# Performance work log

Measured on AMD Instinct MI355X. Metric: run time of the kernel, lower is better.

The kernel has to match this reference:

```python
import jax, jax.numpy as jnp
import numpy as np

T, B, D, H, L = 512, 64, 1024, 1024, 2
W_SCALE = 0.02  # keep tanh out of saturation


def setup_inputs() -> dict:
    key = jax.random.key(0)
    ks = jax.random.split(key, 7)
    return {
        "x": jax.random.normal(ks[0], (T, B, D), dtype=jnp.float32),
        "Wi": jax.random.normal(ks[1], (L, H, D), dtype=jnp.float32) * W_SCALE,
        "bi": jax.random.normal(ks[2], (L, H), dtype=jnp.float32) * W_SCALE,
        "Wh": jax.random.normal(ks[3], (L, H, H), dtype=jnp.float32) * W_SCALE,
        "bh": jax.random.normal(ks[4], (L, H), dtype=jnp.float32) * W_SCALE,
        "Wo": jax.random.normal(ks[5], (L, H, H), dtype=jnp.float32) * W_SCALE,
        "bo": jax.random.normal(ks[6], (L, H), dtype=jnp.float32) * W_SCALE,
    }


def reference(x, Wi, bi, Wh, bh, Wo, bo):
    # Faithful to the original: ONE hidden state shared across all layers,
    # overwritten by each RNNCell call within a timestep.
    num_layers = Wi.shape[0]
    batch = x.shape[1]
    hidden0 = jnp.zeros((batch, Wh.shape[-1]), dtype=x.dtype)

    def step(hidden, xt):
        out = xt
        for l in range(num_layers):
            # h = i2h(out) + h2h(hidden); o = h2o(h); new hidden = tanh(h)
            h = out @ Wi[l].T + bi[l] + hidden @ Wh[l].T + bh[l]  # [B,H]
            out = h @ Wo[l].T + bo[l]
            hidden = jnp.tanh(h)
        return hidden, out

    final_hidden, outs = jax.lax.scan(step, hidden0, x)  # outs: [T,B,H]
    return outs, final_hidden
```

## Files before the change

### kernel.cpp

```cpp
#include <hip/hip_runtime.h>
#include <cstdint>
#include <cstddef>

#define TT   512
#define NWG  256
#define SLOT 65536
#define SLOTB 262144
#define FINALOFF ((size_t)TT * (size_t)SLOT)

#define OFF_M     0
#define OFF_H0    2097152
#define OFF_TH0   (OFF_H0 + 131072)
#define OFF_TH1   (OFF_TH0 + 131072)
#define OFF_H1A   (OFF_TH1 + 131072)
#define OFF_H1B   (OFF_H1A + 131072)
#define OFF_B0    (OFF_H1B + 131072)
#define OFF_C1    (OFF_B0 + 4096)
#define OFF_FLAGS (OFF_C1 + 4096)

typedef _Float16 f16;
typedef unsigned long long ull;
typedef _Float16 v8h __attribute__((ext_vector_type(8)));
typedef float v4f __attribute__((ext_vector_type(4)));

union U2 { ull u[2]; v8h v; };
union P4 { f16 h[4]; ull u; };

__device__ __forceinline__ void st2(void* p, f16 v) {
  __hip_atomic_store((unsigned short*)p, __builtin_bit_cast(unsigned short, v),
                     __ATOMIC_RELAXED, __HIP_MEMORY_SCOPE_AGENT);
}
__device__ __forceinline__ ull ld8(const void* p) {
  return __hip_atomic_load((const ull*)p, __ATOMIC_RELAXED, __HIP_MEMORY_SCOPE_AGENT);
}
__device__ __forceinline__ void ld_frags(const f16* base, v8h out[8]) {
  ull u0[8], u1[8];
#pragma unroll
  for (int s = 0; s < 8; ++s) { const f16* p = base + s * 32; u0[s] = ld8(p); u1[s] = ld8(p + 4); }
#pragma unroll
  for (int s = 0; s < 8; ++s) { U2 c; c.u[0] = u0[s]; c.u[1] = u1[s]; out[s] = c.v; }
}

__device__ __forceinline__ float rcpf(float x) {
#if __has_builtin(__builtin_amdgcn_rcpf)
  return __builtin_amdgcn_rcpf(x);
#else
  return 1.0f / x;
#endif
}
__device__ __forceinline__ float tanhfast(float x) {
  x = fminf(fmaxf(x, -20.0f), 20.0f);
  const float u = __expf(-2.0f * x);
  return 1.0f - 2.0f * u * rcpf(1.0f + u);
}

__global__ void k_init(unsigned int* flags) {
  flags[threadIdx.x] = 0u;
}

__global__ void k_bias(const float* __restrict__ Wi, const float* __restrict__ bi,
                       const float* __restrict__ bh, const float* __restrict__ bo,
                       float* __restrict__ b0, float* __restrict__ c1) {
  const int i = blockIdx.x * 256 + threadIdx.x;
  const float* row = Wi + 1048576 + (size_t)i * 1024;
  float s = 0.f;
  for (int k = 0; k < 1024; k += 4) {
    const float4 w = *(const float4*)&row[k];
    const float4 v = *(const float4*)&bo[k];
    s += w.x * v.x + w.y * v.y + w.z * v.z + w.w * v.w;
  }
  c1[i] = s + bi[1024 + i] + bh[1024 + i];
  b0[i] = bi[i] + bh[i];
}

__global__ __launch_bounds__(256) void k_gemm_M(const float* __restrict__ Wi,
                                                const float* __restrict__ Wo,
                                                f16* __restrict__ Mh) {
  const float* A = Wi + 1048576;
  const float* B = Wo;
  __shared__ float As[16][68];
  __shared__ float Bs[16][68];
  const int bi = blockIdx.x >> 4, bj = blockIdx.x & 15;
  const int i0 = bi * 64, d0 = bj * 64;
  const int ti = threadIdx.x >> 4, tj = threadIdx.x & 15;
  float acc[4][4] = {};
  for (int kc = 0; kc < 1024; kc += 16) {
    const int r = threadIdx.x >> 2, cg = (threadIdx.x & 3) << 2;
    const float4 av = *(const float4*)&A[(size_t)(i0 + r) * 1024 + kc + cg];
    As[cg + 0][r] = av.x; As[cg + 1][r] = av.y; As[cg + 2][r] = av.z; As[cg + 3][r] = av.w;
    const int c2 = threadIdx.x >> 4, dg = (threadIdx.x & 15) << 2;
    const float4 bv = *(const float4*)&B[(size_t)(kc + c2) * 1024 + d0 + dg];
    *(float4*)&Bs[c2][dg] = bv;
    __syncthreads();
#pragma unroll
    for (int kk = 0; kk < 16; ++kk) {
      float a[4], b[4];
#pragma unroll
      for (int q = 0; q < 4; ++q) { a[q] = As[kk][ti * 4 + q]; b[q] = Bs[kk][tj * 4 + q]; }
#pragma unroll
      for (int p = 0; p < 4; ++p)
#pragma unroll
        for (int q = 0; q < 4; ++q) acc[p][q] += a[p] * b[q];
    }
    __syncthreads();
  }
#pragma unroll
  for (int p = 0; p < 4; ++p)
#pragma unroll
    for (int q = 0; q < 4; ++q)
      Mh[(size_t)(i0 + ti * 4 + p) * 1024 + (size_t)(d0 + tj * 4 + q)] = (f16)acc[p][q];
}

__global__ __launch_bounds__(256, 1) void k_z1(const float* __restrict__ x,
                                               const float* __restrict__ Wi,
                                               const float* __restrict__ b0p,
                                               float* __restrict__ dout) {
  const int t = blockIdx.x;
  const int tid = threadIdx.x, l = tid & 63, w = tid >> 6;
  const int lj = l & 15, lk = l >> 4;
  __shared__ __align__(16) f16 XL[64 * 1032];
  const float* xt = x + (size_t)t * SLOT;
  for (int u = tid; u < 16384; u += 256) {
    const int b = u >> 8, c4 = (u & 255) << 2;
    const float4 v = *(const float4*)&xt[(size_t)b * 1024 + c4];
    P4 p; p.h[0] = (f16)v.x; p.h[1] = (f16)v.y; p.h[2] = (f16)v.z; p.h[3] = (f16)v.w;
    *(ull*)&XL[b * 1032 + c4] = p.u;
  }
  __syncthreads();
  for (int jt = 0; jt < 16; ++jt) {
    const int jb = w * 256 + jt * 16;
    v4f acc[4] = {{0.f,0.f,0.f,0.f},{0.f,0.f,0.f,0.f},{0.f,0.f,0.f,0.f},{0.f,0.f,0.f,0.f}};
    for (int ks = 0; ks < 32; ++ks) {
      const int k0 = ks * 32 + lk * 8;
      const float* p = &Wi[(size_t)(jb + lj) * 1024 + k0];
      const float4 a = *(const float4*)p, b = *(const float4*)(p + 4);
      const v8h wf = {(f16)a.x,(f16)a.y,(f16)a.z,(f16)a.w,
                      (f16)b.x,(f16)b.y,(f16)b.z,(f16)b.w};
#pragma unroll
      for (int bt = 0; bt < 4; ++bt) {
        const v8h xf = *(const v8h*)&XL[(bt * 16 + lj) * 1032 + k0];
        acc[bt] = __builtin_amdgcn_mfma_f32_16x16x32_f16(xf, wf, acc[bt], 0, 0, 0);
      }
    }
    const float bias = b0p[jb + lj];
#pragma unroll
    for (int bt = 0; bt < 4; ++bt)
#pragma unroll
      for (int q = 0; q < 4; ++q) {
        const int b = bt * 16 + lk * 4 + q;
        f16* dst = (f16*)((char*)dout + (size_t)t * SLOTB + (size_t)(b >> 4) * 65536
                          + (size_t)(b & 15) * 2048) + (jb + lj);
        *dst = (f16)(acc[bt][q] + bias);
      }
  }
}

__global__ __launch_bounds__(256, 1) void k_rnn(
    const float* __restrict__ Wh, const float* __restrict__ Wo,
    const float* __restrict__ bo,
    char* __restrict__ ws, float* __restrict__ dout)
{
  const f16* Mh = (const f16*)(ws + OFF_M);
  f16* h0h  = (f16*)(ws + OFF_H0);
  f16* th0h = (f16*)(ws + OFF_TH0);
  f16* th1h = (f16*)(ws + OFF_TH1);
  f16* h1r[2] = { (f16*)(ws + OFF_H1A), (f16*)(ws + OFF_H1B) };
  const float* c1p = (const float*)(ws + OFF_C1);
  unsigned int* flags = (unsigned int*)(ws + OFF_FLAGS);

  const int wg = blockIdx.x;
  const int bq = wg & 3;
  const int jt = wg >> 2;
  const int j0 = jt * 16;
  const int tid = threadIdx.x;
  const int l = tid & 63, w = tid >> 6;
  const int lj = l & 15, lk = l >> 4;
  const int rb = tid >> 4, rj = tid & 15;
  unsigned int* gf = flags + bq * 64;

  __shared__ __align__(16) char WLb[4 * 32768];
  __shared__ float red[1024];

  {
    const float* srcs[3] = { Wh, Wh + 1048576, Wo + 1048576 };
    const int mi[3] = { 0, 2, 3 };
#pragma unroll
    for (int m = 0; m < 3; ++m) {
      const float* src = srcs[m];
      for (int u = tid; u < 4096; u += 256) {
        const int j = u >> 8, c4 = (u & 255) << 2;
        const float4 v = *(const float4*)&src[(size_t)(j0 + j) * 1024 + c4];
        P4 p; p.h[0] = (f16)v.x; p.h[1] = (f16)v.y; p.h[2] = (f16)v.z; p.h[3] = (f16)v.w;
        *(ull*)(WLb + mi[m] * 32768 + ((c4 >> 3) << 8) + (j << 4) + ((c4 & 4) << 1)) = p.u;
      }
    }
    for (int u = tid; u < 2048; u += 256) {
      const int j = u >> 7, c8 = (u & 127) << 3;
      const v8h mv = *(const v8h*)&Mh[(size_t)(j0 + j) * 1024 + c8];
      *(v8h*)(WLb + 32768 + ((c8 >> 3) << 8) + (j << 4)) = mv;
    }
  }
  const float c1v = c1p[j0 + rj];
  const float bo1v = bo[1024 + j0 + rj];
  __syncthreads();

  const size_t actbase = (size_t)(bq * 16 + lj) * 1024 + (size_t)(w * 256 + lk * 8);
  const int redw = w * 256 + lk * 64 + lj;
  const size_t rdst = (size_t)(bq * 16 + rb) * 1024 + (size_t)(j0 + rj);
  const int fbase = ((w * 32 + lk) << 8) + (lj << 4);

  auto wfrag = [&](int m, int s) -> v8h {
    return *(const v8h*)(WLb + m * 32768 + fbase + (s << 10));
  };
  auto zptr = [&](int t) -> const f16* {
    return (const f16*)((const char*)dout + (size_t)t * SLOTB + (size_t)bq * 65536
                        + (size_t)rb * 2048) + (j0 + rj);
  };
  auto reduce4 = [&](v4f a) -> float {
    __syncthreads();
#pragma unroll
    for (int q = 0; q < 4; ++q) red[redw + q * 16] = a[q];
    __syncthreads();
    return red[tid] + red[256 + tid] + red[512 + tid] + red[768 + tid];
  };
  auto arrive = [&](unsigned int ph) {
    asm volatile("s_waitcnt vmcnt(0)" ::: "memory");
    __syncthreads();
    if (tid == 0)
      __hip_atomic_store(&gf[jt], ph, __ATOMIC_RELAXED, __HIP_MEMORY_SCOPE_AGENT);
  };
  auto wait = [&](unsigned int ph) {
    if (tid < 64)
      while (__hip_atomic_load(&gf[tid], __ATOMIC_RELAXED, __HIP_MEMORY_SCOPE_AGENT) < ph)
        __builtin_amdgcn_s_sleep(1);
    __syncthreads();
    asm volatile("" ::: "memory");
  };

  float zv = (float)(*zptr(0));
  unsigned int ph = 0;
  v4f a2 = {0.f, 0.f, 0.f, 0.f};

  for (int t = 0; t < TT; ++t) {
    v8h hrf[8];
    v4f accA = {0.f, 0.f, 0.f, 0.f};
    if (t > 0) {
      v8h thf[8];
      ld_frags(th1h + actbase, thf);
      ld_frags(h1r[(t - 1) & 1] + actbase, hrf);
#pragma unroll
      for (int s = 0; s < 8; ++s)
        accA = __builtin_amdgcn_mfma_f32_16x16x32_f16(thf[s], wfrag(0, s), accA, 0, 0, 0);
    }
    const float h0 = reduce4(accA) + zv;
    st2(&h0h[rdst], (f16)h0);
    st2(&th0h[rdst], (f16)tanhfast(h0));
    arrive(++ph);
    float zn = 0.f;
    if (t + 1 < TT) zn = (float)(*zptr(t + 1));
    if (t > 0) {
      v4f aa = {0.f, 0.f, 0.f, 0.f};
#pragma unroll
      for (int s = 0; s < 8; ++s)
        aa = __builtin_amdgcn_mfma_f32_16x16x32_f16(hrf[s], wfrag(3, s), aa, 0, 0, 0);
      a2 = aa;
    }
    wait(ph);

    v8h g0f[8], t0f[8];
    ld_frags(h0h + actbase, g0f);
    ld_frags(th0h + actbase, t0f);
    v4f aM = {0.f, 0.f, 0.f, 0.f}, aW = {0.f, 0.f, 0.f, 0.f};
#pragma unroll
    for (int s = 0; s < 8; ++s) {
      aM = __builtin_amdgcn_mfma_f32_16x16x32_f16(g0f[s], wfrag(1, s), aM, 0, 0, 0);
      aW = __builtin_amdgcn_mfma_f32_16x16x32_f16(t0f[s], wfrag(2, s), aW, 0, 0, 0);
    }
    const float h1 = reduce4(aM + aW) + c1v;
    const float th1v = tanhfast(h1);
    st2(&h1r[t & 1][rdst], (f16)h1);
    st2(&th1h[rdst], (f16)th1v);
    if (t == TT - 1) dout[FINALOFF + rdst] = th1v;
    arrive(++ph);
    if (t > 0)
      dout[(size_t)(t - 1) * SLOT + rdst] = reduce4(a2) + bo1v;
    wait(ph);
    zv = zn;
  }

  {
    v8h hrf[8];
    ld_frags(h1r[(TT - 1) & 1] + actbase, hrf);
    v4f aa = {0.f, 0.f, 0.f, 0.f};
#pragma unroll
    for (int s = 0; s < 8; ++s)
      aa = __builtin_amdgcn_mfma_f32_16x16x32_f16(hrf[s], wfrag(3, s), aa, 0, 0, 0);
    dout[(size_t)(TT - 1) * SLOT + rdst] = reduce4(aa) + bo1v;
  }
}

extern "C" void kernel_launch(void* const* d_in, const int* in_sizes, int n_in,
                              void* d_out, int out_size, void* d_ws, size_t ws_size,
                              hipStream_t stream) {
  (void)in_sizes; (void)n_in; (void)out_size; (void)ws_size;
  const float* x  = (const float*)d_in[0];
  const float* Wi = (const float*)d_in[1];
  const float* bi = (const float*)d_in[2];
  const float* Wh = (const float*)d_in[3];
  const float* bh = (const float*)d_in[4];
  const float* Wo = (const float*)d_in[5];
  const float* bo = (const float*)d_in[6];
  char* ws = (char*)d_ws;
  float* out = (float*)d_out;

  k_init<<<1, 256, 0, stream>>>((unsigned int*)(ws + OFF_FLAGS));
  k_bias<<<4, 256, 0, stream>>>(Wi, bi, bh, bo, (float*)(ws + OFF_B0), (float*)(ws + OFF_C1));
  k_gemm_M<<<256, 256, 0, stream>>>(Wi, Wo, (f16*)(ws + OFF_M));
  k_z1<<<512, 256, 0, stream>>>(x, Wi, (const float*)(ws + OFF_B0), out);
  k_rnn<<<NWG, 256, 0, stream>>>(Wh, Wo, bo, ws, out);
}
```

Before: 6.255 ms.

## Repartition persistent RNN into 8-column tiles with counter barriers and blocked activations

Each workgroup now owns 8 hidden columns across two batch quarters instead of 16 columns of one quarter. The activation buffers move to a blocked layout so each tile's output is one contiguous 256-byte chunk. The per-workgroup flag array polled by 64 threads is replaced by atomic arrival counters polled by a single load. The aim is to cut the cost of the per-step grid barrier and to make activation stores and loads contiguous. In exchange, half of each MFMA tile is wasted on zero weight fragments, only half the threads do useful reduction work, and there are more reduction syncs per step.

```diff
diff --git a/kernel.cpp b/kernel.cpp
--- a/kernel.cpp
+++ b/kernel.cpp
@@ -8,15 +8,15 @@
 #define SLOTB 262144
 #define FINALOFF ((size_t)TT * (size_t)SLOT)
 
-#define OFF_M     0
-#define OFF_H0    2097152
-#define OFF_TH0   (OFF_H0 + 131072)
-#define OFF_TH1   (OFF_TH0 + 131072)
-#define OFF_H1A   (OFF_TH1 + 131072)
-#define OFF_H1B   (OFF_H1A + 131072)
-#define OFF_B0    (OFF_H1B + 131072)
-#define OFF_C1    (OFF_B0 + 4096)
-#define OFF_FLAGS (OFF_C1 + 4096)
+#define OFF_M    0
+#define XB_H0    2097152
+#define XB_TH0   (XB_H0 + 131072)
+#define XB_TH1   (XB_TH0 + 131072)
+#define XB_H1A   (XB_TH1 + 131072)
+#define XB_H1B   (XB_H1A + 131072)
+#define OFF_B0   (XB_H1B + 131072)
+#define OFF_C1   (OFF_B0 + 4096)
+#define OFF_CNT  (OFF_C1 + 4096)
 
 typedef _Float16 f16;
 typedef unsigned long long ull;
@@ -30,13 +30,25 @@
   __hip_atomic_store((unsigned short*)p, __builtin_bit_cast(unsigned short, v),
                      __ATOMIC_RELAXED, __HIP_MEMORY_SCOPE_AGENT);
 }
+__device__ __forceinline__ f16 ld2(const void* p) {
+  unsigned short u = __hip_atomic_load((const unsigned short*)p,
+                                       __ATOMIC_RELAXED, __HIP_MEMORY_SCOPE_AGENT);
+  return __builtin_bit_cast(f16, u);
+}
 __device__ __forceinline__ ull ld8(const void* p) {
   return __hip_atomic_load((const ull*)p, __ATOMIC_RELAXED, __HIP_MEMORY_SCOPE_AGENT);
 }
-__device__ __forceinline__ void ld_frags(const f16* base, v8h out[8]) {
+__device__ __forceinline__ void cadd(unsigned int* c) {
+  __hip_atomic_fetch_add(c, 1u, __ATOMIC_RELAXED, __HIP_MEMORY_SCOPE_AGENT);
+}
+__device__ __forceinline__ void cpoll(const unsigned int* c, unsigned int tgt) {
+  while (__hip_atomic_load(c, __ATOMIC_RELAXED, __HIP_MEMORY_SCOPE_AGENT) < tgt) {}
+}
+
+__device__ __forceinline__ void ld_frags8(const f16* base, v8h out[8]) {
   ull u0[8], u1[8];
 #pragma unroll
-  for (int s = 0; s < 8; ++s) { const f16* p = base + s * 32; u0[s] = ld8(p); u1[s] = ld8(p + 4); }
+  for (int s = 0; s < 8; ++s) { const f16* p = base + s * 512; u0[s] = ld8(p); u1[s] = ld8(p + 4); }
 #pragma unroll
   for (int s = 0; s < 8; ++s) { U2 c; c.u[0] = u0[s]; c.u[1] = u1[s]; out[s] = c.v; }
 }
@@ -54,8 +66,8 @@
   return 1.0f - 2.0f * u * rcpf(1.0f + u);
 }
 
-__global__ void k_init(unsigned int* flags) {
-  flags[threadIdx.x] = 0u;
+__global__ void k_init(unsigned int* cnt) {
+  cnt[threadIdx.x] = 0u;
 }
 
 __global__ void k_bias(const float* __restrict__ Wi, const float* __restrict__ bi,
@@ -127,8 +139,8 @@
     *(ull*)&XL[b * 1032 + c4] = p.u;
   }
   __syncthreads();
-  for (int jt = 0; jt < 16; ++jt) {
-    const int jb = w * 256 + jt * 16;
+  for (int jtile = 0; jtile < 16; ++jtile) {
+    const int jb = w * 256 + jtile * 16;
     v4f acc[4] = {{0.f,0.f,0.f,0.f},{0.f,0.f,0.f,0.f},{0.f,0.f,0.f,0.f},{0.f,0.f,0.f,0.f}};
     for (int ks = 0; ks < 32; ++ks) {
       const int k0 = ks * 32 + lk * 8;
@@ -143,13 +155,15 @@
       }
     }
     const float bias = b0p[jb + lj];
+    const int jt8 = w * 32 + jtile * 2 + (lj >> 3);
+    const int jr = lj & 7;
 #pragma unroll
     for (int bt = 0; bt < 4; ++bt)
 #pragma unroll
       for (int q = 0; q < 4; ++q) {
-        const int b = bt * 16 + lk * 4 + q;
-        f16* dst = (f16*)((char*)dout + (size_t)t * SLOTB + (size_t)(b >> 4) * 65536
-                          + (size_t)(b & 15) * 2048) + (jb + lj);
+        const int bp = lk * 4 + q;
+        f16* dst = (f16*)((char*)dout + (size_t)t * SLOTB + (size_t)bt * 65536
+                          + (size_t)jt8 * 256) + bp * 8 + jr;
         *dst = (f16)(acc[bt][q] + bias);
       }
   }
@@ -161,25 +175,27 @@
     char* __restrict__ ws, float* __restrict__ dout)
 {
   const f16* Mh = (const f16*)(ws + OFF_M);
-  f16* h0h  = (f16*)(ws + OFF_H0);
-  f16* th0h = (f16*)(ws + OFF_TH0);
-  f16* th1h = (f16*)(ws + OFF_TH1);
-  f16* h1r[2] = { (f16*)(ws + OFF_H1A), (f16*)(ws + OFF_H1B) };
+  f16* h0B  = (f16*)(ws + XB_H0);
+  f16* th0B = (f16*)(ws + XB_TH0);
+  f16* th1B = (f16*)(ws + XB_TH1);
+  f16* h1B[2] = { (f16*)(ws + XB_H1A), (f16*)(ws + XB_H1B) };
   const float* c1p = (const float*)(ws + OFF_C1);
-  unsigned int* flags = (unsigned int*)(ws + OFF_FLAGS);
+  unsigned int* cnt = (unsigned int*)(ws + OFF_CNT);
 
   const int wg = blockIdx.x;
-  const int bq = wg & 3;
-  const int jt = wg >> 2;
-  const int j0 = jt * 16;
+  const int pm = wg & 1;
+  const int q0 = pm * 2, q1 = q0 + 1;
+  const int jt = wg >> 1;
+  const int j0 = jt * 8;
   const int tid = threadIdx.x;
   const int l = tid & 63, w = tid >> 6;
   const int lj = l & 15, lk = l >> 4;
-  const int rb = tid >> 4, rj = tid & 15;
-  unsigned int* gf = flags + bq * 64;
-
-  __shared__ __align__(16) char WLb[4 * 32768];
-  __shared__ float red[1024];
+
+  unsigned int* cA0 = cnt + q0 * 64; unsigned int* cB0 = cA0 + 32;
+  unsigned int* cA1 = cnt + q1 * 64; unsigned int* cB1 = cA1 + 32;
+
+  __shared__ __align__(16) f16 WL[4 * 8192];
+  __shared__ float red[5120];
 
   {
     const float* srcs[3] = { Wh, Wh + 1048576, Wo + 1048576 };
@@ -187,115 +203,174 @@
 #pragma unroll
     for (int m = 0; m < 3; ++m) {
       const float* src = srcs[m];
-      for (int u = tid; u < 4096; u += 256) {
+      const int mo = mi[m] * 8192;
+      for (int u = tid; u < 2048; u += 256) {
         const int j = u >> 8, c4 = (u & 255) << 2;
         const float4 v = *(const float4*)&src[(size_t)(j0 + j) * 1024 + c4];
         P4 p; p.h[0] = (f16)v.x; p.h[1] = (f16)v.y; p.h[2] = (f16)v.z; p.h[3] = (f16)v.w;
-        *(ull*)(WLb + mi[m] * 32768 + ((c4 >> 3) << 8) + (j << 4) + ((c4 & 4) << 1)) = p.u;
-      }
-    }
-    for (int u = tid; u < 2048; u += 256) {
+        *(ull*)&WL[mo + ((c4 >> 3) << 6) + (j << 3) + (c4 & 7)] = p.u;
+      }
+    }
+    for (int u = tid; u < 1024; u += 256) {
       const int j = u >> 7, c8 = (u & 127) << 3;
-      const v8h mv = *(const v8h*)&Mh[(size_t)(j0 + j) * 1024 + c8];
-      *(v8h*)(WLb + 32768 + ((c8 >> 3) << 8) + (j << 4)) = mv;
-    }
-  }
-  const float c1v = c1p[j0 + rj];
-  const float bo1v = bo[1024 + j0 + rj];
+      *(v8h*)&WL[8192 + ((c8 >> 3) << 6) + (j << 3)] = *(const v8h*)&Mh[(size_t)(j0 + j) * 1024 + c8];
+    }
+  }
+  const bool act = (tid < 128);
+  const int rb = tid >> 3, rj = tid & 7;
+  float c1v = 0.f, bo1v = 0.f;
+  if (act) { c1v = c1p[j0 + rj]; bo1v = bo[1024 + j0 + rj]; }
   __syncthreads();
 
-  const size_t actbase = (size_t)(bq * 16 + lj) * 1024 + (size_t)(w * 256 + lk * 8);
+  const int xb = (w * 32 + lk) * 128 + lj * 8;
+  const int xs = jt * 128 + tid;
   const int redw = w * 256 + lk * 64 + lj;
-  const size_t rdst = (size_t)(bq * 16 + rb) * 1024 + (size_t)(j0 + rj);
-  const int fbase = ((w * 32 + lk) << 8) + (lj << 4);
 
   auto wfrag = [&](int m, int s) -> v8h {
-    return *(const v8h*)(WLb + m * 32768 + fbase + (s << 10));
-  };
-  auto zptr = [&](int t) -> const f16* {
-    return (const f16*)((const char*)dout + (size_t)t * SLOTB + (size_t)bq * 65536
-                        + (size_t)rb * 2048) + (j0 + rj);
+    v8h r = {};
+    if (lj < 8) r = *(const v8h*)&WL[m * 8192 + (w * 32 + s * 4 + lk) * 64 + lj * 8];
+    return r;
   };
   auto reduce4 = [&](v4f a) -> float {
     __syncthreads();
 #pragma unroll
     for (int q = 0; q < 4; ++q) red[redw + q * 16] = a[q];
     __syncthreads();
-    return red[tid] + red[256 + tid] + red[512 + tid] + red[768 + tid];
+    float r = 0.f;
+    if (act) { const int sl = rb * 16 + rj; r = red[sl] + red[256 + sl] + red[512 + sl] + red[768 + sl]; }
+    return r;
   };
-  auto arrive = [&](unsigned int ph) {
+  auto zaddr = [&](int t, int q) -> const f16* {
+    return (const f16*)((const char*)dout + (size_t)t * SLOTB + (size_t)q * 65536 + (size_t)jt * 256);
+  };
+
+  float zv0 = 0.f, zv1 = 0.f;
+  if (act) { zv0 = (float)ld2(zaddr(0, q0) + tid); zv1 = (float)ld2(zaddr(0, q1) + tid); }
+
+  v4f a2q0 = {0.f,0.f,0.f,0.f}, a2q1 = {0.f,0.f,0.f,0.f};
+
+  for (int t = 0; t < TT; ++t) {
+    const bool R = (t > 0);
+    {
+      v4f acc = {0.f,0.f,0.f,0.f};
+      if (R) {
+        v8h thf[8]; ld_frags8(th1B + q0 * 16384 + xb, thf);
+#pragma unroll
+        for (int s = 0; s < 8; ++s)
+          acc = __builtin_amdgcn_mfma_f32_16x16x32_f16(thf[s], wfrag(0, s), acc, 0, 0, 0);
+      }
+      const float h0 = reduce4(acc) + zv0;
+      if (act) { st2(&h0B[q0 * 16384 + xs], (f16)h0); st2(&th0B[q0 * 16384 + xs], (f16)tanhfast(h0)); }
+    }
+    {
+      v4f acc = {0.f,0.f,0.f,0.f};
+      if (R) {
+        v8h thf[8]; ld_frags8(th1B + q1 * 16384 + xb, thf);
+#pragma unroll
+        for (int s = 0; s < 8; ++s)
+          acc = __builtin_amdgcn_mfma_f32_16x16x32_f16(thf[s], wfrag(0, s), acc, 0, 0, 0);
+      }
+      const float h0 = reduce4(acc) + zv1;
+      if (act) { st2(&h0B[q1 * 16384 + xs], (f16)h0); st2(&th0B[q1 * 16384 + xs], (f16)tanhfast(h0)); }
+    }
     asm volatile("s_waitcnt vmcnt(0)" ::: "memory");
     __syncthreads();
-    if (tid == 0)
-      __hip_atomic_store(&gf[jt], ph, __ATOMIC_RELAXED, __HIP_MEMORY_SCOPE_AGENT);
-  };
-  auto wait = [&](unsigned int ph) {
-    if (tid < 64)
-      while (__hip_atomic_load(&gf[tid], __ATOMIC_RELAXED, __HIP_MEMORY_SCOPE_AGENT) < ph)
-        __builtin_amdgcn_s_sleep(1);
-    __syncthreads();
+    if (tid == 0) { cadd(cA0); cadd(cA1); }
     asm volatile("" ::: "memory");
-  };
-
-  float zv = (float)(*zptr(0));
-  unsigned int ph = 0;
-  v4f a2 = {0.f, 0.f, 0.f, 0.f};
-
-  for (int t = 0; t < TT; ++t) {
-    v8h hrf[8];
-    v4f accA = {0.f, 0.f, 0.f, 0.f};
-    if (t > 0) {
-      v8h thf[8];
-      ld_frags(th1h + actbase, thf);
-      ld_frags(h1r[(t - 1) & 1] + actbase, hrf);
-#pragma unroll
-      for (int s = 0; s < 8; ++s)
-        accA = __builtin_amdgcn_mfma_f32_16x16x32_f16(thf[s], wfrag(0, s), accA, 0, 0, 0);
-    }
-    const float h0 = reduce4(accA) + zv;
-    st2(&h0h[rdst], (f16)h0);
-    st2(&th0h[rdst], (f16)tanhfast(h0));
-    arrive(++ph);
-    float zn = 0.f;
-    if (t + 1 < TT) zn = (float)(*zptr(t + 1));
-    if (t > 0) {
-      v4f aa = {0.f, 0.f, 0.f, 0.f};
+
+    float zn0 = 0.f, zn1 = 0.f;
+    if (t + 1 < TT && act) {
+      zn0 = (float)ld2(zaddr(t + 1, q0) + tid);
+      zn1 = (float)ld2(zaddr(t + 1, q1) + tid);
+      asm volatile("" : "+v"(zn0), "+v"(zn1));
+    }
+    if (R) {
+      v8h hrf[8];
+      ld_frags8(h1B[(t - 1) & 1] + q0 * 16384 + xb, hrf);
+      v4f aa = {0.f,0.f,0.f,0.f};
 #pragma unroll
       for (int s = 0; s < 8; ++s)
         aa = __builtin_amdgcn_mfma_f32_16x16x32_f16(hrf[s], wfrag(3, s), aa, 0, 0, 0);
-      a2 = aa;
-    }
-    wait(ph);
-
-    v8h g0f[8], t0f[8];
-    ld_frags(h0h + actbase, g0f);
-    ld_frags(th0h + actbase, t0f);
-    v4f aM = {0.f, 0.f, 0.f, 0.f}, aW = {0.f, 0.f, 0.f, 0.f};
-#pragma unroll
-    for (int s = 0; s < 8; ++s) {
-      aM = __builtin_amdgcn_mfma_f32_16x16x32_f16(g0f[s], wfrag(1, s), aM, 0, 0, 0);
-      aW = __builtin_amdgcn_mfma_f32_16x16x32_f16(t0f[s], wfrag(2, s), aW, 0, 0, 0);
-    }
-    const float h1 = reduce4(aM + aW) + c1v;
-    const float th1v = tanhfast(h1);
-    st2(&h1r[t & 1][rdst], (f16)h1);
-    st2(&th1h[rdst], (f16)th1v);
-    if (t == TT - 1) dout[FINALOFF + rdst] = th1v;
-    arrive(++ph);
-    if (t > 0)
-      dout[(size_t)(t - 1) * SLOT + rdst] = reduce4(a2) + bo1v;
-    wait(ph);
-    zv = zn;
+      a2q0 = aa;
+      ld_frags8(h1B[(t - 1) & 1] + q1 * 16384 + xb, hrf);
+      aa = (v4f){0.f,0.f,0.f,0.f};
+#pragma unroll
+      for (int s = 0; s < 8; ++s)
+        aa = __builtin_amdgcn_mfma_f32_16x16x32_f16(hrf[s], wfrag(3, s), aa, 0, 0, 0);
+      a2q1 = aa;
+      asm volatile("" : "+v"(a2q0), "+v"(a2q1));
+    }
+
+    cpoll(cA0, 128u * (unsigned)(t + 1));
+    {
+      v8h g0f[8], t0f[8];
+      ld_frags8(h0B + q0 * 16384 + xb, g0f);
+      ld_frags8(th0B + q0 * 16384 + xb, t0f);
+      v4f aM = {0.f,0.f,0.f,0.f}, aW = {0.f,0.f,0.f,0.f};
+#pragma unroll
+      for (int s = 0; s < 8; ++s) {
+        aM = __builtin_amdgcn_mfma_f32_16x16x32_f16(g0f[s], wfrag(1, s), aM, 0, 0, 0);
+        aW = __builtin_amdgcn_mfma_f32_16x16x32_f16(t0f[s], wfrag(2, s), aW, 0, 0, 0);
+      }
+      const float h1 = reduce4(aM + aW) + c1v;
+      if (act) {
+        const float th1v = tanhfast(h1);
+        st2(&h1B[t & 1][q0 * 16384 + xs], (f16)h1);
+        st2(&th1B[q0 * 16384 + xs], (f16)th1v);
+        if (t == TT - 1) dout[FINALOFF + (size_t)(q0 * 16 + rb) * 1024 + j0 + rj] = th1v;
+      }
+    }
+    cpoll(cA1, 128u * (unsigned)(t + 1));
+    {
+      v8h g0f[8], t0f[8];
+      ld_frags8(h0B + q1 * 16384 + xb, g0f);
+      ld_frags8(th0B + q1 * 16384 + xb, t0f);
+      v4f aM = {0.f,0.f,0.f,0.f}, aW = {0.f,0.f,0.f,0.f};
+#pragma unroll
+      for (int s = 0; s < 8; ++s) {
+        aM = __builtin_amdgcn_mfma_f32_16x16x32_f16(g0f[s], wfrag(1, s), aM, 0, 0, 0);
+        aW = __builtin_amdgcn_mfma_f32_16x16x32_f16(t0f[s], wfrag(2, s), aW, 0, 0, 0);
+      }
+      const float h1 = reduce4(aM + aW) + c1v;
+      if (act) {
+        const float th1v = tanhfast(h1);
+        st2(&h1B[t & 1][q1 * 16384 + xs], (f16)h1);
+        st2(&th1B[q1 * 16384 + xs], (f16)th1v);
+        if (t == TT - 1) dout[FINALOFF + (size_t)(q1 * 16 + rb) * 1024 + j0 + rj] = th1v;
+      }
+    }
+    asm volatile("s_waitcnt vmcnt(0)" ::: "memory");
+    __syncthreads();
+    if (tid == 0) { cadd(cB0); cadd(cB1); }
+    asm volatile("" ::: "memory");
+
+    if (R) {
+      const float o0 = reduce4(a2q0) + bo1v;
+      if (act) dout[(size_t)(t - 1) * SLOT + (size_t)(q0 * 16 + rb) * 1024 + j0 + rj] = o0;
+      const float o1 = reduce4(a2q1) + bo1v;
+      if (act) dout[(size_t)(t - 1) * SLOT + (size_t)(q1 * 16 + rb) * 1024 + j0 + rj] = o1;
+    }
+    cpoll(cB0, 128u * (unsigned)(t + 1));
+    cpoll(cB1, 128u * (unsigned)(t + 1));
+    zv0 = zn0; zv1 = zn1;
   }
 
   {
     v8h hrf[8];
-    ld_frags(h1r[(TT - 1) & 1] + actbase, hrf);
-    v4f aa = {0.f, 0.f, 0.f, 0.f};
+    ld_frags8(h1B[(TT - 1) & 1] + q0 * 16384 + xb, hrf);
+    v4f aa = {0.f,0.f,0.f,0.f};
 #pragma unroll
     for (int s = 0; s < 8; ++s)
       aa = __builtin_amdgcn_mfma_f32_16x16x32_f16(hrf[s], wfrag(3, s), aa, 0, 0, 0);
-    dout[(size_t)(TT - 1) * SLOT + rdst] = reduce4(aa) + bo1v;
+    const float o0 = reduce4(aa) + bo1v;
+    if (act) dout[(size_t)(TT - 1) * SLOT + (size_t)(q0 * 16 + rb) * 1024 + j0 + rj] = o0;
+    ld_frags8(h1B[(TT - 1) & 1] + q1 * 16384 + xb, hrf);
+    aa = (v4f){0.f,0.f,0.f,0.f};
+#pragma unroll
+    for (int s = 0; s < 8; ++s)
+      aa = __builtin_amdgcn_mfma_f32_16x16x32_f16(hrf[s], wfrag(3, s), aa, 0, 0, 0);
+    const float o1 = reduce4(aa) + bo1v;
+    if (act) dout[(size_t)(TT - 1) * SLOT + (size_t)(q1 * 16 + rb) * 1024 + j0 + rj] = o1;
   }
 }
 
@@ -313,7 +388,7 @@
   char* ws = (char*)d_ws;
   float* out = (float*)d_out;
 
-  k_init<<<1, 256, 0, stream>>>((unsigned int*)(ws + OFF_FLAGS));
+  k_init<<<1, 256, 0, stream>>>((unsigned int*)(ws + OFF_CNT));
   k_bias<<<4, 256, 0, stream>>>(Wi, bi, bh, bo, (float*)(ws + OFF_B0), (float*)(ws + OFF_C1));
   k_gemm_M<<<256, 256, 0, stream>>>(Wi, Wo, (f16*)(ws + OFF_M));
   k_z1<<<512, 256, 0, stream>>>(x, Wi, (const float*)(ws + OFF_B0), out);
```

After: 7.674 ms. 22.7% more time.

## Overlap loads with grid barriers using partial vmcnt waits and reordered output work

Applied to the files above, without the earlier changes.

Replaces the arrive/wait barrier pair with a flag set preceded by a partial s_waitcnt vmcnt. Only this block's own stores must complete before it signals, so the next step's fragment loads can stay in flight across the barrier. The th1 fragment load is prefetched after the second barrier. The h2o output projection and its reduction now run before the first poll, which is meant to hide barrier latency. The hardcoded vmcnt counts depend on the exact instruction ordering the compiler emits, so a compiler change could break memory ordering.

```diff
diff --git a/kernel.cpp b/kernel.cpp
--- a/kernel.cpp
+++ b/kernel.cpp
@@ -223,31 +223,26 @@
     __syncthreads();
     return red[tid] + red[256 + tid] + red[512 + tid] + red[768 + tid];
   };
-  auto arrive = [&](unsigned int ph) {
-    asm volatile("s_waitcnt vmcnt(0)" ::: "memory");
-    __syncthreads();
-    if (tid == 0)
-      __hip_atomic_store(&gf[jt], ph, __ATOMIC_RELAXED, __HIP_MEMORY_SCOPE_AGENT);
-  };
-  auto wait = [&](unsigned int ph) {
+  auto pollge = [&](unsigned int ph) {
     if (tid < 64)
       while (__hip_atomic_load(&gf[tid], __ATOMIC_RELAXED, __HIP_MEMORY_SCOPE_AGENT) < ph)
         __builtin_amdgcn_s_sleep(1);
     __syncthreads();
     asm volatile("" ::: "memory");
   };
+  auto setflag = [&](unsigned int ph) {
+    if (tid == 0)
+      __hip_atomic_store(&gf[jt], ph, __ATOMIC_RELAXED, __HIP_MEMORY_SCOPE_AGENT);
+  };
 
   float zv = (float)(*zptr(0));
-  unsigned int ph = 0;
-  v4f a2 = {0.f, 0.f, 0.f, 0.f};
+  v8h thf[8];
 
   for (int t = 0; t < TT; ++t) {
-    v8h hrf[8];
+    const bool R = (t > 0);
+
     v4f accA = {0.f, 0.f, 0.f, 0.f};
-    if (t > 0) {
-      v8h thf[8];
-      ld_frags(th1h + actbase, thf);
-      ld_frags(h1r[(t - 1) & 1] + actbase, hrf);
+    if (R) {
 #pragma unroll
       for (int s = 0; s < 8; ++s)
         accA = __builtin_amdgcn_mfma_f32_16x16x32_f16(thf[s], wfrag(0, s), accA, 0, 0, 0);
@@ -255,17 +250,28 @@
     const float h0 = reduce4(accA) + zv;
     st2(&h0h[rdst], (f16)h0);
     st2(&th0h[rdst], (f16)tanhfast(h0));
-    arrive(++ph);
+
+    v8h hrf[8];
+    if (R) ld_frags(h1r[(t - 1) & 1] + actbase, hrf);
     float zn = 0.f;
     if (t + 1 < TT) zn = (float)(*zptr(t + 1));
-    if (t > 0) {
+
+    if (t == 0)            { asm volatile("s_waitcnt vmcnt(1)"  ::: "memory"); }
+    else if (t == TT - 1)  { asm volatile("s_waitcnt vmcnt(16)" ::: "memory"); }
+    else                   { asm volatile("s_waitcnt vmcnt(17)" ::: "memory"); }
+    __syncthreads();
+    setflag(2u * t + 1u);
+
+    float oval = 0.f;
+    if (R) {
+      asm volatile("s_waitcnt vmcnt(0)" ::: "memory");
       v4f aa = {0.f, 0.f, 0.f, 0.f};
 #pragma unroll
       for (int s = 0; s < 8; ++s)
         aa = __builtin_amdgcn_mfma_f32_16x16x32_f16(hrf[s], wfrag(3, s), aa, 0, 0, 0);
-      a2 = aa;
-    }
-    wait(ph);
+      oval = reduce4(aa) + bo1v;
+    }
+    pollge(2u * t + 1u);
 
     v8h g0f[8], t0f[8];
     ld_frags(h0h + actbase, g0f);
@@ -280,11 +286,17 @@
     const float th1v = tanhfast(h1);
     st2(&h1r[t & 1][rdst], (f16)h1);
     st2(&th1h[rdst], (f16)th1v);
+    if (R) dout[(size_t)(t - 1) * SLOT + rdst] = oval;
     if (t == TT - 1) dout[FINALOFF + rdst] = th1v;
-    arrive(++ph);
-    if (t > 0)
-      dout[(size_t)(t - 1) * SLOT + rdst] = reduce4(a2) + bo1v;
-    wait(ph);
+
+    if (t == 0)            { asm volatile("s_waitcnt vmcnt(0)" ::: "memory"); }
+    else if (t == TT - 1)  { asm volatile("s_waitcnt vmcnt(2)" ::: "memory"); }
+    else                   { asm volatile("s_waitcnt vmcnt(1)" ::: "memory"); }
+    __syncthreads();
+    setflag(2u * t + 2u);
+    pollge(2u * t + 2u);
+
+    if (t + 1 < TT) ld_frags(th1h + actbase, thf);
     zv = zn;
   }
 
```

Measured after the change: 6.856 ms. 1.1x slower.
